# Kernel tuning notes

Measured on AMD Instinct MI355X. Metric: run time of the kernel, lower is better.

Reference implementation:

```python
import jax, jax.numpy as jnp
import numpy as np

H_HEADS = 32
KV_HEADS = 8
HEAD_DIM = 64  # hidden // num_heads = 2048 // 32


def setup_inputs() -> dict:
    key = jax.random.key(0)
    ks = jax.random.split(key, 5)
    B, T, hidden = 2, 2048, 2048
    kv_dim = KV_HEADS * HEAD_DIM
    s = 0.02
    return {
        "x": jax.random.normal(ks[0], (B, T, hidden), dtype=jnp.float32),
        "Wq": jax.random.normal(ks[1], (hidden, hidden), dtype=jnp.float32) * s,
        "Wk": jax.random.normal(ks[2], (hidden, kv_dim), dtype=jnp.float32) * s,
        "Wv": jax.random.normal(ks[3], (hidden, kv_dim), dtype=jnp.float32) * s,
        "Wo": jax.random.normal(ks[4], (hidden, hidden), dtype=jnp.float32) * s,
    }


def reference(x, Wq, Wk, Wv, Wo):
    B, T, hidden = x.shape
    h, kv, d = H_HEADS, KV_HEADS, HEAD_DIM
    g = h // kv  # GQA group size
    scale = d ** (-0.5)

    # projections
    q = (x @ Wq).reshape(B, T, h, d).transpose(0, 2, 1, 3)        # [B,h,T,d]
    k = (x @ Wk).reshape(B, T, kv, d).transpose(0, 2, 1, 3)      # [B,kv,T,d]
    v = (x @ Wv).reshape(B, T, kv, d).transpose(0, 2, 1, 3)      # [B,kv,T,d]

    # native GQA broadcast: group q heads by their shared kv head
    # (equivalent math to torch repeat_interleave on k/v)
    qg = q.reshape(B, kv, g, T, d)                                # [B,kv,g,T,d]
    scores = jnp.einsum("bkgtd,bksd->bkgts", qg, k) * scale       # [B,kv,g,T,T]
    attn = jax.nn.softmax(scores, axis=-1)
    og = jnp.einsum("bkgts,bksd->bkgtd", attn, v)                 # [B,kv,g,T,d]
    out = og.reshape(B, h, T, d).transpose(0, 2, 1, 3).reshape(B, T, h * d)
    return out @ Wo
```

## Files before the change

### kernel.cpp

```cpp
#include <hip/hip_runtime.h>

#define AS1 __attribute__((address_space(1)))
#define AS3 __attribute__((address_space(3)))

typedef unsigned short u16;
typedef unsigned int u32;
typedef __attribute__((ext_vector_type(8))) _Float16 half8;
typedef __attribute__((ext_vector_type(2))) _Float16 half2v;
typedef __attribute__((ext_vector_type(4))) u16 u16x4;
typedef __attribute__((ext_vector_type(4))) u32 u32x4;
typedef __attribute__((ext_vector_type(4))) float f32x4;
typedef __attribute__((ext_vector_type(16))) float f32x16;

__device__ __forceinline__ u16 f2h(float f) {
    _Float16 h = (_Float16)f;
    return __builtin_bit_cast(u16, h);
}

__device__ __forceinline__ u32 pk2h(float a, float b) {
    return __builtin_bit_cast(u32, __builtin_amdgcn_cvt_pkrtz(a, b));
}

__device__ __forceinline__ float fexp2(float x) {
#if __has_builtin(__builtin_amdgcn_exp2f)
    return __builtin_amdgcn_exp2f(x);
#else
    return __expf(x * 0.69314718055994531f);
#endif
}

__device__ __forceinline__ float dot2acc(u32 w, float acc) {
#if __has_builtin(__builtin_amdgcn_fdot2)
    half2v ones = { (_Float16)1.f, (_Float16)1.f };
    return __builtin_amdgcn_fdot2(__builtin_bit_cast(half2v, w), ones, acc, false);
#else
    half2v p = __builtin_bit_cast(half2v, w);
    return acc + (float)p[0] + (float)p[1];
#endif
}

__device__ __forceinline__ void plswap(u32& a, u32& b) {
    asm("v_permlane32_swap_b32 %0, %1" : "+v"(a), "+v"(b));
}

__device__ __forceinline__ void async16(const void* g, void* l) {
    __builtin_amdgcn_global_load_lds((AS1 void*)g, (AS3 void*)l, 16, 0, 0);
}


__global__ void cast_f32_to_f16(const float* __restrict__ in, u16* __restrict__ out) {
    int i = (blockIdx.x * 256 + threadIdx.x) * 4;
    float4 v = *(const float4*)(in + i);
    u16x4 o = { f2h(v.x), f2h(v.y), f2h(v.z), f2h(v.w) };
    *(u16x4*)(out + i) = o;
}

__global__ void transpose_cast4(const float* __restrict__ Wq, const float* __restrict__ Wk,
                                const float* __restrict__ Wv, const float* __restrict__ Wo,
                                u16* __restrict__ Wqt, u16* __restrict__ Wkvt,
                                u16* __restrict__ Wot, float qscale) {
    __shared__ float tile[32][33];
    const int z = blockIdx.z;
    const float* in;
    u16* out;
    int N;
    float scale = 1.f;
    if (z == 0)      { in = Wq; out = Wqt; N = 2048; scale = qscale; }
    else if (z == 1) { in = Wo; out = Wot; N = 2048; }
    else if (z == 2) { in = Wk; out = Wkvt; N = 512; }
    else             { in = Wv; out = Wkvt + (size_t)512 * 2048; N = 512; }
    const int K = 2048;
    int nb = blockIdx.x * 32, kb = blockIdx.y * 32;
    if (nb >= N) return;
    int tx = threadIdx.x & 31, ty = threadIdx.x >> 5;
#pragma unroll
    for (int r = ty; r < 32; r += 8)
        tile[r][tx] = in[(size_t)(kb + r) * N + nb + tx];
    __syncthreads();
#pragma unroll
    for (int r = ty; r < 32; r += 8)
        out[(size_t)(nb + r) * K + kb + tx] = f2h(tile[tx][r] * scale);
}


template <int OUTMODE>
__global__ __launch_bounds__(256, OUTMODE == 3 ? 3 : 2) void gemm_bt(
        const u16* __restrict__ A, const u16* __restrict__ Bt,
        void* __restrict__ C, void* __restrict__ C2,
        int M, int N, int K, int ldc) {
    __shared__ __align__(16) u16 As[2][128 * 32];
    __shared__ __align__(16) u16 Bs[2][128 * 32];
    const int m0 = blockIdx.x * 128, n0 = blockIdx.y * 128;
    const int wave = threadIdx.x >> 6, lane = threadIdx.x & 63;
    const int quad = lane >> 4, mm = lane & 15;
    const int wm = (wave >> 1) * 64, wn = (wave & 1) * 64;

    const int srow = wave * 16 + (lane >> 2);
    const int scol = 8 * ((lane & 3) ^ ((lane >> 3) & 3));

    const u16* ag0 = A + (size_t)(m0 + srow) * K + scol;
    const u16* ag1 = A + (size_t)(m0 + 64 + srow) * K + scol;
    const u16* bg0 = Bt + (size_t)(n0 + srow) * K + scol;
    const u16* bg1 = Bt + (size_t)(n0 + 64 + srow) * K + scol;
    const int soff = wave * 512 + lane * 8;

    f32x4 acc[4][4] = {};
    const int swz = (mm >> 1) & 3;

#define GST(buf)                                                              \
    {                                                                         \
        u16* ad = &As[buf][soff];                                             \
        u16* bd = &Bs[buf][soff];                                             \
        async16(ag0, ad);                                                     \
        async16(ag1, ad + 2048);                                              \
        async16(bg0, bd);                                                     \
        async16(bg1, bd + 2048);                                              \
        ag0 += 32; ag1 += 32; bg0 += 32; bg1 += 32;                           \
    }

    GST(0);
    int cur = 0;

    for (int k0 = 0; k0 < K; k0 += 32) {
        __syncthreads();
        if (k0 + 32 < K) GST(cur ^ 1);
        const u16* Ac = &As[cur][0];
        const u16* Bc = &Bs[cur][0];
        half8 af[4], bf[4];
#pragma unroll
        for (int i = 0; i < 4; i++)
            af[i] = *(const half8*)(Ac + (wm + i * 16 + mm) * 32 + (quad ^ swz) * 8);
#pragma unroll
        for (int i = 0; i < 4; i++)
            bf[i] = *(const half8*)(Bc + (wn + i * 16 + mm) * 32 + (quad ^ swz) * 8);
#pragma unroll
        for (int mi = 0; mi < 4; mi++)
#pragma unroll
            for (int ni = 0; ni < 4; ni++)
                acc[mi][ni] = __builtin_amdgcn_mfma_f32_16x16x32_f16(
                    af[mi], bf[ni], acc[mi][ni], 0, 0, 0);
        cur ^= 1;
    }
#undef GST

    if (OUTMODE == 0) {
        float* Cp = (float*)C;
#pragma unroll
        for (int mi = 0; mi < 4; mi++)
#pragma unroll
            for (int r = 0; r < 4; r++) {
                float* rp = Cp + (size_t)(m0 + wm + mi * 16 + quad * 4 + r) * ldc + n0 + wn + mm;
#pragma unroll
                for (int ni = 0; ni < 4; ni++) rp[ni * 16] = acc[mi][ni][r];
            }
    } else if (OUTMODE == 1) {
        u16* Cp = (u16*)C;
#pragma unroll
        for (int mi = 0; mi < 4; mi++)
#pragma unroll
            for (int r = 0; r < 4; r++) {
                u16* rp = Cp + (size_t)(m0 + wm + mi * 16 + quad * 4 + r) * ldc + n0 + wn + mm;
#pragma unroll
                for (int ni = 0; ni < 4; ni++) rp[ni * 16] = f2h(acc[mi][ni][r]);
            }
    } else if (OUTMODE == 2) {
        u16* Cp = (u16*)C;
#pragma unroll
        for (int mi = 0; mi < 4; mi++)
#pragma unroll
            for (int r = 0; r < 4; r++) {
                int row = m0 + wm + mi * 16 + quad * 4 + r;
#pragma unroll
                for (int ni = 0; ni < 4; ni++)
                    Cp[(size_t)(n0 + wn + ni * 16 + mm) * ldc + row] = f2h(acc[mi][ni][r]);
            }
    } else {
        if (n0 < 2048) {
            u16* Qp = (u16*)C;
#pragma unroll
            for (int mi = 0; mi < 4; mi++)
#pragma unroll
                for (int r = 0; r < 4; r++) {
                    u16* rp = Qp + (size_t)(m0 + wm + mi * 16 + quad * 4 + r) * 2048 + n0 + wn + mm;
#pragma unroll
                    for (int ni = 0; ni < 4; ni++) rp[ni * 16] = f2h(acc[mi][ni][r]);
                }
        } else if (n0 < 2560) {
            u16* Kp = (u16*)C2;
#pragma unroll
            for (int mi = 0; mi < 4; mi++)
#pragma unroll
                for (int r = 0; r < 4; r++) {
                    u16* rp = Kp + (size_t)(m0 + wm + mi * 16 + quad * 4 + r) * 512 + (n0 - 2048) + wn + mm;
#pragma unroll
                    for (int ni = 0; ni < 4; ni++) rp[ni * 16] = f2h(acc[mi][ni][r]);
                }
        } else {
            u16* Vp = (u16*)C2 + (size_t)4096 * 512;
#pragma unroll
            for (int mi = 0; mi < 4; mi++)
#pragma unroll
                for (int r = 0; r < 4; r++) {
                    int row = m0 + wm + mi * 16 + quad * 4 + r;
#pragma unroll
                    for (int ni = 0; ni < 4; ni++)
                        Vp[(size_t)(n0 - 2560 + wn + ni * 16 + mm) * 4096 + row] = f2h(acc[mi][ni][r]);
                }
        }
    }
}


template <int SPLIT>
__global__ __launch_bounds__(256, 4) void attn_fwd(const u16* __restrict__ Qb,
                                                   const u16* __restrict__ Kb,
                                                   const u16* __restrict__ Vtb,
                                                   u16* __restrict__ Ob,
                                                   float* __restrict__ Of0,
                                                   float* __restrict__ Of1,
                                                   float* __restrict__ Lf) {
    __shared__ __align__(16) u16 Ks[2][64 * 64];
    __shared__ __align__(16) u16 Vs[2][64 * 64];

    const int qtb = blockIdx.x, head = blockIdx.y;
    const int b = blockIdx.z & 1, sp = blockIdx.z >> 1;
    const int kvh = head >> 2;
    const int wave = threadIdx.x >> 6, lane = threadIdx.x & 63;
    const int h = lane >> 5;
    const int q32 = lane & 31;
    const int t = threadIdx.x;

    const size_t qrow0 = (size_t)b * 2048 + qtb * 128 + wave * 32;
    const int s_beg = sp * (2048 / SPLIT), s_end = s_beg + 2048 / SPLIT;

    half8 qf[4];
#pragma unroll
    for (int s = 0; s < 4; s++)
        qf[s] = *(const half8*)(Qb + (qrow0 + q32) * 2048 + head * 64 + s * 16 + h * 8);

    f32x16 accO[2] = {};
    float lpq[4] = {0.f, 0.f, 0.f, 0.f};

    f32x16 NEG10;
#pragma unroll
    for (int i = 0; i < 16; i++) NEG10[i] = -10.f;

    const int srow = t >> 3;
    const int lch = (t & 7) ^ (srow & 7);
    const u16* kg = Kb + ((size_t)b * 2048 + srow) * 512 + kvh * 64 + lch * 8;
    const u16* vg = Vtb + ((size_t)kvh * 64 + srow) * 4096 + b * 2048 + lch * 8;

#define STAGE(buf, s0)                                                        \
    {                                                                         \
        u16* kd = &Ks[buf][t * 8];                                            \
        u16* vd = &Vs[buf][t * 8];                                            \
        async16(kg + (size_t)(s0) * 512, kd);                                 \
        async16(kg + (size_t)((s0) + 32) * 512, kd + 2048);                   \
        async16(vg + (s0), vd);                                               \
        async16(vg + (size_t)32 * 4096 + (s0), vd + 2048);                    \
    }

    int cur = 0;
    STAGE(0, s_beg);

    const int r0 = q32, r1 = 32 + q32;
    const int sw0 = (r0 & 7), sw1 = (r1 & 7);

    for (int s0 = s_beg; s0 < s_end; s0 += 64) {
        __syncthreads();
        int sn = s0 + 64;
        if (sn < s_end) STAGE(cur ^ 1, sn);

        const u16* Kc = &Ks[cur][0];
        const u16* Vc = &Vs[cur][0];
        const u16* Kr0 = Kc + r0 * 64;
        const u16* Kr1 = Kc + r1 * 64;

        f32x16 a0, a1;
        __builtin_amdgcn_s_setprio(1);
        {
            half8 k0 = *(const half8*)(Kr0 + ((h ^ sw0) << 3));
            a0 = __builtin_amdgcn_mfma_f32_32x32x16_f16(k0, qf[0], NEG10, 0, 0, 0);
            half8 k1 = *(const half8*)(Kr1 + ((h ^ sw1) << 3));
            a1 = __builtin_amdgcn_mfma_f32_32x32x16_f16(k1, qf[0], NEG10, 0, 0, 0);
        }
#pragma unroll
        for (int s = 1; s < 4; s++) {
            half8 k0 = *(const half8*)(Kr0 + (((2 * s + h) ^ sw0) << 3));
            a0 = __builtin_amdgcn_mfma_f32_32x32x16_f16(k0, qf[s], a0, 0, 0, 0);
            half8 k1 = *(const half8*)(Kr1 + (((2 * s + h) ^ sw1) << 3));
            a1 = __builtin_amdgcn_mfma_f32_32x32x16_f16(k1, qf[s], a1, 0, 0, 0);
        }
        __builtin_amdgcn_s_setprio(0);

        u32 w0[8];
#pragma unroll
        for (int m = 0; m < 8; m++) {
            w0[m] = pk2h(fexp2(a0[2 * m]), fexp2(a0[2 * m + 1]));
            lpq[m & 3] = dot2acc(w0[m], lpq[m & 3]);
        }

        __builtin_amdgcn_s_setprio(1);
#pragma unroll
        for (int k1 = 0; k1 < 2; k1++) {
            const int ks = k1;
            u32 d0 = w0[4 * k1 + 0], d2 = w0[4 * k1 + 2];
            u32 d1 = w0[4 * k1 + 1], d3 = w0[4 * k1 + 3];
            plswap(d0, d2);
            plswap(d1, d3);
            u32x4 pd = { d0, d1, d2, d3 };
            half8 pf = __builtin_bit_cast(half8, pd);
#pragma unroll
            for (int dt = 0; dt < 2; dt++) {
                const int rv = dt * 32 + q32;
                half8 vf = *(const half8*)(&Vc[rv * 64 + (((2 * ks + h) ^ (rv & 7)) << 3)]);
                accO[dt] = __builtin_amdgcn_mfma_f32_32x32x16_f16(vf, pf, accO[dt], 0, 0, 0);
            }
        }
        __builtin_amdgcn_s_setprio(0);

        u32 w1[8];
#pragma unroll
        for (int m = 0; m < 8; m++) {
            w1[m] = pk2h(fexp2(a1[2 * m]), fexp2(a1[2 * m + 1]));
            lpq[m & 3] = dot2acc(w1[m], lpq[m & 3]);
        }

        __builtin_amdgcn_s_setprio(1);
#pragma unroll
        for (int k1 = 0; k1 < 2; k1++) {
            const int ks = 2 + k1;
            u32 d0 = w1[4 * k1 + 0], d2 = w1[4 * k1 + 2];
            u32 d1 = w1[4 * k1 + 1], d3 = w1[4 * k1 + 3];
            plswap(d0, d2);
            plswap(d1, d3);
            u32x4 pd = { d0, d1, d2, d3 };
            half8 pf = __builtin_bit_cast(half8, pd);
#pragma unroll
            for (int dt = 0; dt < 2; dt++) {
                const int rv = dt * 32 + q32;
                half8 vf = *(const half8*)(&Vc[rv * 64 + (((2 * ks + h) ^ (rv & 7)) << 3)]);
                accO[dt] = __builtin_amdgcn_mfma_f32_32x32x16_f16(vf, pf, accO[dt], 0, 0, 0);
            }
        }
        __builtin_amdgcn_s_setprio(0);

        cur ^= 1;
    }
#undef STAGE

    float l = (lpq[0] + lpq[1]) + (lpq[2] + lpq[3]);
    l += __shfl_xor(l, 32);

    const size_t token = qrow0 + q32;
    if (SPLIT == 1) {
        float inv = 1.f / l;
#pragma unroll
        for (int dt = 0; dt < 2; dt++)
#pragma unroll
            for (int rq = 0; rq < 4; rq++) {
                u16x4 o = { f2h(accO[dt][4 * rq + 0] * inv), f2h(accO[dt][4 * rq + 1] * inv),
                            f2h(accO[dt][4 * rq + 2] * inv), f2h(accO[dt][4 * rq + 3] * inv) };
                *(u16x4*)(Ob + token * 2048 + head * 64 + dt * 32 + rq * 8 + h * 4) = o;
            }
    } else {
        float* Op = sp ? Of1 : Of0;
#pragma unroll
        for (int dt = 0; dt < 2; dt++)
#pragma unroll
            for (int rq = 0; rq < 4; rq++) {
                f32x4 o = { accO[dt][4 * rq + 0], accO[dt][4 * rq + 1],
                            accO[dt][4 * rq + 2], accO[dt][4 * rq + 3] };
                *(f32x4*)(Op + token * 2048 + head * 64 + dt * 32 + rq * 8 + h * 4) = o;
            }
        if (!h) Lf[((size_t)sp * 4096 + token) * 32 + head] = l;
    }
}


extern "C" void kernel_launch(void* const* d_in, const int* in_sizes, int n_in,
                              void* d_out, int out_size, void* d_ws, size_t ws_size,
                              hipStream_t stream) {
    (void)in_sizes; (void)n_in; (void)out_size; (void)ws_size;
    const float* x  = (const float*)d_in[0];
    const float* Wq = (const float*)d_in[1];
    const float* Wk = (const float*)d_in[2];
    const float* Wv = (const float*)d_in[3];
    const float* Wo = (const float*)d_in[4];
    float* out = (float*)d_out;

    u16* ws = (u16*)d_ws;
    u16* xb   = ws;
    u16* Wqt  = xb   + (size_t)4096 * 2048;
    u16* Wkvt = Wqt  + (size_t)2048 * 2048;
    u16* Wot  = Wkvt + (size_t)1024 * 2048;
    u16* Qb   = Wot  + (size_t)2048 * 2048;
    u16* Kb   = Qb   + (size_t)4096 * 2048;
    u16* Vtb  = Kb   + (size_t)4096 * 512;
    u16* Ob   = Vtb  + (size_t)512 * 4096;

    const float qscale = 0.125f * 1.4426950408889634f;

    cast_f32_to_f16<<<8192, 256, 0, stream>>>(x, xb);
    transpose_cast4<<<dim3(64, 64, 4), 256, 0, stream>>>(Wq, Wk, Wv, Wo,
                                                         Wqt, Wkvt, Wot, qscale);

    gemm_bt<3><<<dim3(32, 24), 256, 0, stream>>>(xb, Wqt, Qb, Kb, 4096, 3072, 2048, 2048);

    attn_fwd<1><<<dim3(16, 32, 2), 256, 0, stream>>>(Qb, Kb, Vtb, Ob,
                                                     nullptr, nullptr, nullptr);

    gemm_bt<0><<<dim3(32, 16), 256, 0, stream>>>(Ob, Wot, out, nullptr, 4096, 2048, 2048, 2048);
}
```

Measured before the change: 313.9 us.

## Fuse input prep kernels, vectorize transposed stores, widen attention blocks to 512 threads

The x cast is merged into the weight transpose/cast kernel as an extra grid slice, removing one launch. The transposed V and OUTMODE 2 stores now write four consecutive fp16 rows as a single 8-byte vector instead of scalar stores. The attention kernel runs 512 threads per block covering 256 query rows, so each thread stages one K and one V chunk and a K/V tile in LDS is shared by twice as many query rows. This halves the attention grid and raises per-block register pressure under the new launch bounds.

```diff
diff --git a/kernel.cpp b/kernel.cpp
--- a/kernel.cpp
+++ b/kernel.cpp
@@ -8,6 +8,7 @@
 typedef __attribute__((ext_vector_type(8))) _Float16 half8;
 typedef __attribute__((ext_vector_type(2))) _Float16 half2v;
 typedef __attribute__((ext_vector_type(4))) u16 u16x4;
+typedef __attribute__((ext_vector_type(8))) u16 u16x8;
 typedef __attribute__((ext_vector_type(4))) u32 u32x4;
 typedef __attribute__((ext_vector_type(4))) float f32x4;
 typedef __attribute__((ext_vector_type(16))) float f32x16;
@@ -48,19 +49,22 @@
 }
 
 
-__global__ void cast_f32_to_f16(const float* __restrict__ in, u16* __restrict__ out) {
-    int i = (blockIdx.x * 256 + threadIdx.x) * 4;
-    float4 v = *(const float4*)(in + i);
-    u16x4 o = { f2h(v.x), f2h(v.y), f2h(v.z), f2h(v.w) };
-    *(u16x4*)(out + i) = o;
-}
-
-__global__ void transpose_cast4(const float* __restrict__ Wq, const float* __restrict__ Wk,
-                                const float* __restrict__ Wv, const float* __restrict__ Wo,
-                                u16* __restrict__ Wqt, u16* __restrict__ Wkvt,
-                                u16* __restrict__ Wot, float qscale) {
+__global__ void prep_inputs(const float* __restrict__ x, u16* __restrict__ xb,
+                            const float* __restrict__ Wq, const float* __restrict__ Wk,
+                            const float* __restrict__ Wv, const float* __restrict__ Wo,
+                            u16* __restrict__ Wqt, u16* __restrict__ Wkvt,
+                            u16* __restrict__ Wot, float qscale) {
     __shared__ float tile[32][33];
     const int z = blockIdx.z;
+    if (z == 4) {
+        size_t base = ((size_t)(blockIdx.y * 64 + blockIdx.x) * 256 + threadIdx.x) * 8;
+        float4 v0 = *(const float4*)(x + base);
+        float4 v1 = *(const float4*)(x + base + 4);
+        u16x8 o = { f2h(v0.x), f2h(v0.y), f2h(v0.z), f2h(v0.w),
+                    f2h(v1.x), f2h(v1.y), f2h(v1.z), f2h(v1.w) };
+        *(u16x8*)(xb + base) = o;
+        return;
+    }
     const float* in;
     u16* out;
     int N;
@@ -168,11 +172,12 @@
 #pragma unroll
         for (int mi = 0; mi < 4; mi++)
 #pragma unroll
-            for (int r = 0; r < 4; r++) {
-                int row = m0 + wm + mi * 16 + quad * 4 + r;
-#pragma unroll
-                for (int ni = 0; ni < 4; ni++)
-                    Cp[(size_t)(n0 + wn + ni * 16 + mm) * ldc + row] = f2h(acc[mi][ni][r]);
+            for (int ni = 0; ni < 4; ni++) {
+                int col = n0 + wn + ni * 16 + mm;
+                int row0 = m0 + wm + mi * 16 + quad * 4;
+                u16x4 o = { f2h(acc[mi][ni][0]), f2h(acc[mi][ni][1]),
+                            f2h(acc[mi][ni][2]), f2h(acc[mi][ni][3]) };
+                *(u16x4*)((u16*)Cp + (size_t)col * ldc + row0) = o;
             }
     } else {
         if (n0 < 2048) {
@@ -200,11 +205,12 @@
 #pragma unroll
             for (int mi = 0; mi < 4; mi++)
 #pragma unroll
-                for (int r = 0; r < 4; r++) {
-                    int row = m0 + wm + mi * 16 + quad * 4 + r;
-#pragma unroll
-                    for (int ni = 0; ni < 4; ni++)
-                        Vp[(size_t)(n0 - 2560 + wn + ni * 16 + mm) * 4096 + row] = f2h(acc[mi][ni][r]);
+                for (int ni = 0; ni < 4; ni++) {
+                    int col = n0 - 2560 + wn + ni * 16 + mm;
+                    int row0 = m0 + wm + mi * 16 + quad * 4;
+                    u16x4 o = { f2h(acc[mi][ni][0]), f2h(acc[mi][ni][1]),
+                                f2h(acc[mi][ni][2]), f2h(acc[mi][ni][3]) };
+                    *(u16x4*)(Vp + (size_t)col * 4096 + row0) = o;
                 }
         }
     }
@@ -212,7 +218,7 @@
 
 
 template <int SPLIT>
-__global__ __launch_bounds__(256, 4) void attn_fwd(const u16* __restrict__ Qb,
+__global__ __launch_bounds__(512, 4) void attn_fwd(const u16* __restrict__ Qb,
                                                    const u16* __restrict__ Kb,
                                                    const u16* __restrict__ Vtb,
                                                    u16* __restrict__ Ob,
@@ -230,7 +236,7 @@
     const int q32 = lane & 31;
     const int t = threadIdx.x;
 
-    const size_t qrow0 = (size_t)b * 2048 + qtb * 128 + wave * 32;
+    const size_t qrow0 = (size_t)b * 2048 + qtb * 256 + wave * 32;
     const int s_beg = sp * (2048 / SPLIT), s_end = s_beg + 2048 / SPLIT;
 
     half8 qf[4];
@@ -252,12 +258,8 @@
 
 #define STAGE(buf, s0)                                                        \
     {                                                                         \
-        u16* kd = &Ks[buf][t * 8];                                            \
-        u16* vd = &Vs[buf][t * 8];                                            \
-        async16(kg + (size_t)(s0) * 512, kd);                                 \
-        async16(kg + (size_t)((s0) + 32) * 512, kd + 2048);                   \
-        async16(vg + (s0), vd);                                               \
-        async16(vg + (size_t)32 * 4096 + (s0), vd + 2048);                    \
+        async16(kg + (size_t)(s0) * 512, &Ks[buf][t * 8]);                    \
+        async16(vg + (s0), &Vs[buf][t * 8]);                                  \
     }
 
     int cur = 0;
@@ -401,14 +403,13 @@
 
     const float qscale = 0.125f * 1.4426950408889634f;
 
-    cast_f32_to_f16<<<8192, 256, 0, stream>>>(x, xb);
-    transpose_cast4<<<dim3(64, 64, 4), 256, 0, stream>>>(Wq, Wk, Wv, Wo,
-                                                         Wqt, Wkvt, Wot, qscale);
+    prep_inputs<<<dim3(64, 64, 5), 256, 0, stream>>>(x, xb, Wq, Wk, Wv, Wo,
+                                                     Wqt, Wkvt, Wot, qscale);
 
     gemm_bt<3><<<dim3(32, 24), 256, 0, stream>>>(xb, Wqt, Qb, Kb, 4096, 3072, 2048, 2048);
 
-    attn_fwd<1><<<dim3(16, 32, 2), 256, 0, stream>>>(Qb, Kb, Vtb, Ob,
-                                                     nullptr, nullptr, nullptr);
+    attn_fwd<1><<<dim3(8, 32, 2), 512, 0, stream>>>(Qb, Kb, Vtb, Ob,
+                                                    nullptr, nullptr, nullptr);
 
     gemm_bt<0><<<dim3(32, 16), 256, 0, stream>>>(Ob, Wot, out, nullptr, 4096, 2048, 2048, 2048);
 }
```

New measurement: 315.6 us. About the same (+0.5%).
